# Optimization experiments

Hardware: AMD Instinct MI355X
Metric: run time of the kernel (lower is better)

The kernel has to match this reference:

```python
import math
import jax, jax.numpy as jnp
import numpy as np

B, C, E = 8, 2048, 1024

def setup_inputs() -> dict:
    key = jax.random.key(0)
    ks = jax.random.split(key, 7)
    s_e = 1.0 / math.sqrt(E)
    s_c = 1.0 / math.sqrt(C)
    return {
        'x': jax.random.normal(ks[0], (B, C, E), dtype=jnp.float32),
        'fc_w': jax.random.normal(ks[1], (E, E), dtype=jnp.float32) * s_e,
        'fc_b': jax.random.normal(ks[2], (E,), dtype=jnp.float32) * s_e,
        'alt_fc_w': jax.random.normal(ks[3], (C, C), dtype=jnp.float32) * s_c,
        'alt_fc_b': jax.random.normal(ks[4], (C,), dtype=jnp.float32) * s_c,
        'vfc_w': jax.random.normal(ks[5], (E, E), dtype=jnp.float32) * s_e,
        'vfc_b': jax.random.normal(ks[6], (E,), dtype=jnp.float32) * s_e,
    }

def reference(x, fc_w, fc_b, alt_fc_w, alt_fc_b, vfc_w, vfc_b):
    # y = fc(x): [b,c,e]
    y = jnp.einsum('bce,fe->bcf', x, fc_w) + fc_b
    # yx = alt_fc(x^T): [b,e,c] -> Linear over context dim -> [b,e,k]
    xx = jnp.swapaxes(x, 1, 2)                    # [b,e,c]
    yx = jnp.einsum('bec,kc->bek', xx, alt_fc_w) + alt_fc_b
    # attention scores: [b,c,k]
    attn = jnp.einsum('bce,bek->bck', y, yx)
    scale = 1.0 / math.sqrt(attn.shape[-1])
    attn = jax.nn.softmax(attn * scale, axis=-1)
    # values
    vx = jnp.einsum('bke,fe->bkf', x, vfc_w) + vfc_b
    out = jnp.einsum('bck,bke->bce', attn, vx)
    # post_feed=None -> return y only
    return out
```

## Files before the change

kernel.cpp:

```cpp
#include <hip/hip_runtime.h>
#include <stdint.h>

#define Bb 8
#define Cc 2048
#define Ee 1024

typedef unsigned short u16;
typedef __attribute__((ext_vector_type(8))) short short8;
typedef __attribute__((ext_vector_type(4))) float f32x4;

__device__ __forceinline__ u16 f2bf(float f){
    unsigned u = __builtin_bit_cast(unsigned, f);
    return (u16)((u + 0x7fffu + ((u >> 16) & 1u)) >> 16);
}
__device__ __forceinline__ float bf2f(u16 h){
    return __builtin_bit_cast(float, ((unsigned)h) << 16);
}
__device__ __forceinline__ void gld16(const void* g, void* l){
    __builtin_amdgcn_global_load_lds(
        (const __attribute__((address_space(1))) unsigned int*)g,
        (__attribute__((address_space(3))) unsigned int*)l,
        16, 0, 0);
}
#define MFMA(a,b,c) __builtin_amdgcn_mfma_f32_16x16x32_bf16((a),(b),(c),0,0,0)
#define SBAR()  __builtin_amdgcn_s_barrier()
#define SCHED0() __builtin_amdgcn_sched_barrier(0)
#define LGKM8() asm volatile("s_waitcnt lgkmcnt(8)" ::: "memory")
#define LGKM4() asm volatile("s_waitcnt lgkmcnt(4)" ::: "memory")
#define LGKM0() asm volatile("s_waitcnt lgkmcnt(0)" ::: "memory")
#define VMCNT0() asm volatile("s_waitcnt vmcnt(0)" ::: "memory")

__global__ __launch_bounds__(256) void k_cast_xt(const float* __restrict__ src,
                                                 u16* __restrict__ xb,
                                                 u16* __restrict__ xbT){
    __shared__ float tile[32][33];
    const int b = blockIdx.z;
    src += (long)b * Cc * Ee;
    xb  += (long)b * Cc * Ee;
    xbT += (long)b * Cc * Ee;
    const int c0 = blockIdx.x * 32;
    const int r0 = blockIdx.y * 32;
    const int tx = threadIdx.x & 31;
    const int ty = threadIdx.x >> 5;
    #pragma unroll
    for (int p = 0; p < 4; ++p){
        float v = src[(long)(r0 + ty + p*8) * Ee + c0 + tx];
        tile[ty + p*8][tx] = v;
        xb[(long)(r0 + ty + p*8) * Ee + c0 + tx] = f2bf(v);
    }
    __syncthreads();
    #pragma unroll
    for (int p = 0; p < 4; ++p)
        xbT[(long)(c0 + ty + p*8) * Cc + r0 + tx] = f2bf(tile[tx][ty + p*8]);
}

__global__ __launch_bounds__(256) void k_cast3(const float* __restrict__ s0, u16* __restrict__ d0, long n0,
                                               const float* __restrict__ s1, u16* __restrict__ d1, long n1,
                                               const float* __restrict__ s2, u16* __restrict__ d2, long n2){
    long i = (long)blockIdx.x * 256 + threadIdx.x;
    const long stride = (long)gridDim.x * 256;
    const long tot = n0 + n1 + n2;
    for (; i < tot; i += stride){
        const float* s; u16* d; long k;
        if (i < n0)          { s = s0; d = d0; k = i; }
        else if (i < n0 + n1){ s = s1; d = d1; k = i - n0; }
        else                 { s = s2; d = d2; k = i - n0 - n1; }
        float4 f = ((const float4*)s)[k];
        ((ushort4*)d)[k] = make_ushort4(f2bf(f.x), f2bf(f.y), f2bf(f.z), f2bf(f.w));
    }
}

template<int BIAS_MODE, int OUT_F32, int EPI, int PRIO>
__global__ __launch_bounds__(512, 2)
void k_gemm256(const u16* __restrict__ A, const u16* __restrict__ Bm,
               void* __restrict__ Cout, const float* __restrict__ bias,
               float* __restrict__ extra,
               int N, int K, long sA, long sB, long sC, float scale)
{
    __shared__ __attribute__((aligned(16))) char smem[131072];

    const int gx = gridDim.x, gy = gridDim.y;
    const int nwg = gx * gy * gridDim.z;
    const int lin = blockIdx.x + gx * (blockIdx.y + gy * blockIdx.z);
    const int swz = (lin & 7) * (nwg >> 3) + (lin >> 3);
    const int bx = swz % gx;
    const int tmp = swz / gx;
    const int by = tmp % gy;
    const int bz = tmp / gy;

    A  += (long)bz * sA;
    Bm += (long)bz * sB;
    u16*   Cm = (u16*)Cout + (OUT_F32 ? 0 : (long)bz * sC);
    float* Cf = (float*)Cout + (OUT_F32 ? (long)bz * sC : 0);

    const int tid  = threadIdx.x;
    const int lane = tid & 63;
    const int wave = tid >> 6;
    const int wr = wave >> 2;
    const int wc = wave & 3;
    const int tileM = bx * 256;
    const int tileN = by * 256;

    const int srow   = tid >> 3;
    const int schunk = (tid & 7) ^ (srow & 7);
    const u16* Ag = A  + (long)(tileM + srow) * K + schunk * 8;
    const u16* Bg = Bm + (long)(tileN + srow) * K + schunk * 8;
    const long uK = (long)64 * K;
    const int  ldst = tid * 16;

    const int lrow = lane & 15;
    const int lk   = lane >> 4;
    const int sw   = lrow & 7;
    const int cs0  = ((0 + lk) ^ sw) * 16;
    const int cs1  = ((4 + lk) ^ sw) * 16;
    const int arow0 = (wr*128 + lrow) * 128;
    const int brow0 = 32768 + (wc*64 + lrow) * 128;

    f32x4 acc[8][4];
    #pragma unroll
    for (int m = 0; m < 8; ++m)
        #pragma unroll
        for (int n = 0; n < 4; ++n)
            acc[m][n] = (f32x4){0.f,0.f,0.f,0.f};

    char* sm = smem;
    #pragma unroll
    for (int u = 0; u < 4; ++u) gld16(Bg + u*uK, sm + 32768 + u*8192 + ldst);
    #pragma unroll
    for (int u = 0; u < 4; ++u) gld16(Ag + u*uK, sm + u*8192 + ldst);
    __syncthreads();

    const int NT = K >> 6;
    short8 aE[4], aO[4], bE[4], bO[4];

    for (int t = 0; t < NT; ++t){
        const bool pref = (t + 1) < NT;
        char* cbuf = sm + ((t & 1) << 16);
        char* nbuf = sm + (((t + 1) & 1) << 16);
        const u16* Agt = Ag + (long)(t + 1) * 64;
        const u16* Bgt = Bg + (long)(t + 1) * 64;

        if (pref){
            gld16(Agt + 0*uK, nbuf + 0*8192 + ldst);
            gld16(Agt + 1*uK, nbuf + 1*8192 + ldst);
            gld16(Agt + 2*uK, nbuf + 2*8192 + ldst);
            gld16(Agt + 3*uK, nbuf + 3*8192 + ldst);
            gld16(Bgt + 0*uK, nbuf + 32768 + 0*8192 + ldst);
            gld16(Bgt + 1*uK, nbuf + 32768 + 1*8192 + ldst);
            gld16(Bgt + 2*uK, nbuf + 32768 + 2*8192 + ldst);
            gld16(Bgt + 3*uK, nbuf + 32768 + 3*8192 + ldst);
        }

        #pragma unroll
        for (int m = 0; m < 4; ++m) aE[m] = *(const short8*)(cbuf + arow0 + m*2048 + cs0);
        #pragma unroll
        for (int n = 0; n < 4; ++n) bE[n] = *(const short8*)(cbuf + brow0 + n*2048 + cs0);
        #pragma unroll
        for (int m = 0; m < 4; ++m) aO[m] = *(const short8*)(cbuf + arow0 + (m+4)*2048 + cs0);

        LGKM4(); SCHED0();
        if (PRIO) __builtin_amdgcn_s_setprio(1);
        #pragma unroll
        for (int m = 0; m < 4; ++m)
            #pragma unroll
            for (int n = 0; n < 4; ++n)
                acc[m][n] = MFMA(aE[m], bE[n], acc[m][n]);
        if (PRIO) __builtin_amdgcn_s_setprio(0);

        #pragma unroll
        for (int m = 0; m < 4; ++m) aE[m] = *(const short8*)(cbuf + arow0 + m*2048 + cs1);
        #pragma unroll
        for (int n = 0; n < 4; ++n) bO[n] = *(const short8*)(cbuf + brow0 + n*2048 + cs1);
        LGKM8(); SCHED0();
        if (PRIO) __builtin_amdgcn_s_setprio(1);
        #pragma unroll
        for (int m = 0; m < 4; ++m)
            #pragma unroll
            for (int n = 0; n < 4; ++n)
                acc[m+4][n] = MFMA(aO[m], bE[n], acc[m+4][n]);
        if (PRIO) __builtin_amdgcn_s_setprio(0);

        #pragma unroll
        for (int m = 0; m < 4; ++m) aO[m] = *(const short8*)(cbuf + arow0 + (m+4)*2048 + cs1);
        LGKM4(); SCHED0();
        if (PRIO) __builtin_amdgcn_s_setprio(1);
        #pragma unroll
        for (int m = 0; m < 4; ++m)
            #pragma unroll
            for (int n = 0; n < 4; ++n)
                acc[m][n] = MFMA(aE[m], bO[n], acc[m][n]);
        if (PRIO) __builtin_amdgcn_s_setprio(0);

        LGKM0(); SCHED0();
        if (PRIO) __builtin_amdgcn_s_setprio(1);
        #pragma unroll
        for (int m = 0; m < 4; ++m)
            #pragma unroll
            for (int n = 0; n < 4; ++n)
                acc[m+4][n] = MFMA(aO[m], bO[n], acc[m+4][n]);
        if (PRIO) __builtin_amdgcn_s_setprio(0);

        VMCNT0(); SBAR(); SCHED0();
    }

    const int r0base = tileM + wr*128 + lk*4;
    const int cbase  = tileN + wc*64 + lrow;

    if (EPI == 0){
        #pragma unroll
        for (int m = 0; m < 8; ++m){
            const int r0 = r0base + m*16;
            #pragma unroll
            for (int n = 0; n < 4; ++n){
                const int c = cbase + n*16;
                f32x4 v = acc[m][n];
                #pragma unroll
                for (int j = 0; j < 4; ++j){
                    float val = v[j] * scale;
                    if (BIAS_MODE == 1) val += bias[c];
                    if (BIAS_MODE == 2) val += bias[r0 + j];
                    if (OUT_F32) Cf[(long)(r0 + j) * N + c] = val;
                    else         Cm[(long)(r0 + j) * N + c] = f2bf(val);
                }
            }
        }
    } else if (EPI == 1){
        float* lsum = (float*)smem;
        const int rl0 = wr*128 + lk*4;
        #pragma unroll
        for (int m = 0; m < 8; ++m){
            const int r0 = r0base + m*16;
            #pragma unroll
            for (int j = 0; j < 4; ++j){
                float rp = 0.f;
                #pragma unroll
                for (int n = 0; n < 4; ++n){
                    float e = __expf(acc[m][n][j] * scale);
                    rp += e;
                    Cm[(long)(r0 + j) * N + (cbase + n*16)] = f2bf(e);
                }
                rp += __shfl_xor(rp, 1);
                rp += __shfl_xor(rp, 2);
                rp += __shfl_xor(rp, 4);
                rp += __shfl_xor(rp, 8);
                if (lrow == 0)
                    lsum[(rl0 + m*16 + j)*4 + wc] = rp;
            }
        }
        __syncthreads();
        if (tid < 256){
            float4 v4 = ((const float4*)lsum)[tid];
            extra[((long)bz*Cc + tileM + tid)*8 + by] = v4.x + v4.y + v4.z + v4.w;
        }
    } else {
        #pragma unroll
        for (int m = 0; m < 8; ++m){
            const int r0 = r0base + m*16;
            #pragma unroll
            for (int j = 0; j < 4; ++j){
                const float4* pr = (const float4*)(extra + ((long)bz*Cc + r0 + j)*8);
                float4 pa = pr[0], pb = pr[1];
                float S = pa.x+pa.y+pa.z+pa.w + pb.x+pb.y+pb.z+pb.w;
                const float inv = 1.f / S;
                #pragma unroll
                for (int n = 0; n < 4; ++n)
                    Cf[(long)(r0 + j) * N + (cbase + n*16)] = acc[m][n][j] * inv;
            }
        }
    }
}

extern "C" void kernel_launch(void* const* d_in, const int* in_sizes, int n_in,
                              void* d_out, int out_size, void* d_ws, size_t ws_size,
                              hipStream_t stream)
{
    const float* x     = (const float*)d_in[0];
    const float* fc_w  = (const float*)d_in[1];
    const float* fc_b  = (const float*)d_in[2];
    const float* altw  = (const float*)d_in[3];
    const float* altb  = (const float*)d_in[4];
    const float* vfc_w = (const float*)d_in[5];
    const float* vfc_b = (const float*)d_in[6];
    float* out = (float*)d_out;

    char* ws = (char*)d_ws;
    const size_t nBCE = (size_t)Bb * Cc * Ee;
    u16* xb   = (u16*)(ws);
    u16* xbT  = (u16*)(ws + 2 * nBCE);
    u16* P    = (u16*)(ws);
    u16* y    = (u16*)(ws + 4 * nBCE);
    u16* z    = (u16*)(ws + 6 * nBCE);
    u16* vxT  = (u16*)(ws + 8 * nBCE);
    u16* fcwb = (u16*)(ws + 10 * nBCE);
    u16* vfwb = fcwb + (size_t)Ee * Ee;
    u16* awb  = vfwb + (size_t)Ee * Ee;
    float* rpart = (float*)(ws + 10 * nBCE);

    k_cast_xt<<<dim3(Ee / 32, Cc / 32, Bb), 256, 0, stream>>>(x, xb, xbT);
    k_cast3<<<2048, 256, 0, stream>>>(fc_w, fcwb, (long)Ee * Ee / 4,
                                      vfc_w, vfwb, (long)Ee * Ee / 4,
                                      altw, awb, (long)Cc * Cc / 4);

    const long sBCE = (long)Cc * Ee;
    const long sBCC = (long)Cc * Cc;
    dim3 blk(512);

    k_gemm256<1, 0, 0, 1><<<dim3(Cc/256, Ee/256, Bb), blk, 0, stream>>>(
        xb, fcwb, y, fc_b, nullptr, Ee, Ee, sBCE, 0, sBCE, 1.f);

    k_gemm256<2, 0, 0, 1><<<dim3(Ee/256, Cc/256, Bb), blk, 0, stream>>>(
        vfwb, xb, vxT, vfc_b, nullptr, Cc, Ee, 0, sBCE, sBCE, 1.f);

    k_gemm256<2, 0, 0, 0><<<dim3(Cc/256, Ee/256, Bb), blk, 0, stream>>>(
        awb, xbT, z, altb, nullptr, Ee, Cc, 0, sBCE, sBCE, 1.f);

    k_gemm256<0, 0, 1, 1><<<dim3(Cc/256, Cc/256, Bb), blk, 0, stream>>>(
        y, z, P, nullptr, rpart, Cc, Ee, sBCE, sBCE, sBCC, 0.022097086912079608f);

    k_gemm256<0, 1, 2, 0><<<dim3(Cc/256, Ee/256, Bb), blk, 0, stream>>>(
        P, vxT, out, nullptr, rpart, Ee, Cc, sBCC, sBCE, sBCE, 1.f);
}
```

Baseline: 309.1 us.

## Merge prep casts and batch the three projection GEMMs into one launch

Folds the x cast/transpose kernel and the weight-cast kernel into a single prep launch. The three independent projection GEMMs (alt_fc, fc, vfc) now run as one grouped launch of 768 workgroups driven by a segment descriptor, so there are fewer launches and fewer partially filled waves. The template specialisations are replaced by runtime segment fields, and the s_setprio hints are removed. The row-sum buffer moves so it no longer overlaps the bf16 weight copies. The cost is runtime branching in the epilogue and possibly weaker compiler specialisation.

```diff
diff --git a/kernel.cpp b/kernel.cpp
--- a/kernel.cpp
+++ b/kernel.cpp
@@ -12,9 +12,6 @@
 __device__ __forceinline__ u16 f2bf(float f){
     unsigned u = __builtin_bit_cast(unsigned, f);
     return (u16)((u + 0x7fffu + ((u >> 16) & 1u)) >> 16);
-}
-__device__ __forceinline__ float bf2f(u16 h){
-    return __builtin_bit_cast(float, ((unsigned)h) << 16);
 }
 __device__ __forceinline__ void gld16(const void* g, void* l){
     __builtin_amdgcn_global_load_lds(
@@ -30,68 +27,85 @@
 #define LGKM0() asm volatile("s_waitcnt lgkmcnt(0)" ::: "memory")
 #define VMCNT0() asm volatile("s_waitcnt vmcnt(0)" ::: "memory")
 
-__global__ __launch_bounds__(256) void k_cast_xt(const float* __restrict__ src,
-                                                 u16* __restrict__ xb,
-                                                 u16* __restrict__ xbT){
+struct Seg {
+    const u16* A; const u16* Bm; void* C; const float* bias; float* extra;
+    int N, K, gx, gy;
+    long sA, sB, sC;
+    float scale;
+    int bias_mode;
+    int epi;
+    int out_f32;
+};
+struct Desc { Seg s0, s1, s2; int n0, n1; };
+
+__global__ __launch_bounds__(256) void k_prep(const float* __restrict__ x,
+                                              u16* __restrict__ xb, u16* __restrict__ xbT,
+                                              const float* __restrict__ fw, u16* __restrict__ fwb,
+                                              const float* __restrict__ vw, u16* __restrict__ vwb,
+                                              const float* __restrict__ aw, u16* __restrict__ awb){
     __shared__ float tile[32][33];
-    const int b = blockIdx.z;
-    src += (long)b * Cc * Ee;
-    xb  += (long)b * Cc * Ee;
-    xbT += (long)b * Cc * Ee;
-    const int c0 = blockIdx.x * 32;
-    const int r0 = blockIdx.y * 32;
-    const int tx = threadIdx.x & 31;
-    const int ty = threadIdx.x >> 5;
-    #pragma unroll
-    for (int p = 0; p < 4; ++p){
-        float v = src[(long)(r0 + ty + p*8) * Ee + c0 + tx];
-        tile[ty + p*8][tx] = v;
-        xb[(long)(r0 + ty + p*8) * Ee + c0 + tx] = f2bf(v);
+    const int blk = blockIdx.x;
+    if (blk < 16384){
+        const int cx = blk & 31;
+        const int rest = blk >> 5;
+        const int cy = rest & 63;
+        const int b  = rest >> 6;
+        const float* src = x + (long)b * Cc * Ee;
+        u16* xbp  = xb  + (long)b * Cc * Ee;
+        u16* xbTp = xbT + (long)b * Cc * Ee;
+        const int c0 = cx * 32;
+        const int r0 = cy * 32;
+        const int tx = threadIdx.x & 31;
+        const int ty = threadIdx.x >> 5;
+        #pragma unroll
+        for (int p = 0; p < 4; ++p){
+            float v = src[(long)(r0 + ty + p*8) * Ee + c0 + tx];
+            tile[ty + p*8][tx] = v;
+            xbp[(long)(r0 + ty + p*8) * Ee + c0 + tx] = f2bf(v);
+        }
+        __syncthreads();
+        #pragma unroll
+        for (int p = 0; p < 4; ++p)
+            xbTp[(long)(c0 + ty + p*8) * Cc + r0 + tx] = f2bf(tile[tx][ty + p*8]);
+    } else {
+        const long n0 = (long)Ee * Ee / 4, n1 = n0, n2 = (long)Cc * Cc / 4;
+        long i = (long)(blk - 16384) * 256 + threadIdx.x;
+        const long stride = 2048L * 256;
+        const long tot = n0 + n1 + n2;
+        for (; i < tot; i += stride){
+            const float* s; u16* d; long k;
+            if (i < n0)          { s = fw; d = fwb; k = i; }
+            else if (i < n0 + n1){ s = vw; d = vwb; k = i - n0; }
+            else                 { s = aw; d = awb; k = i - n0 - n1; }
+            float4 f = ((const float4*)s)[k];
+            ((ushort4*)d)[k] = make_ushort4(f2bf(f.x), f2bf(f.y), f2bf(f.z), f2bf(f.w));
+        }
     }
-    __syncthreads();
-    #pragma unroll
-    for (int p = 0; p < 4; ++p)
-        xbT[(long)(c0 + ty + p*8) * Cc + r0 + tx] = f2bf(tile[tx][ty + p*8]);
-}
-
-__global__ __launch_bounds__(256) void k_cast3(const float* __restrict__ s0, u16* __restrict__ d0, long n0,
-                                               const float* __restrict__ s1, u16* __restrict__ d1, long n1,
-                                               const float* __restrict__ s2, u16* __restrict__ d2, long n2){
-    long i = (long)blockIdx.x * 256 + threadIdx.x;
-    const long stride = (long)gridDim.x * 256;
-    const long tot = n0 + n1 + n2;
-    for (; i < tot; i += stride){
-        const float* s; u16* d; long k;
-        if (i < n0)          { s = s0; d = d0; k = i; }
-        else if (i < n0 + n1){ s = s1; d = d1; k = i - n0; }
-        else                 { s = s2; d = d2; k = i - n0 - n1; }
-        float4 f = ((const float4*)s)[k];
-        ((ushort4*)d)[k] = make_ushort4(f2bf(f.x), f2bf(f.y), f2bf(f.z), f2bf(f.w));
-    }
-}
-
-template<int BIAS_MODE, int OUT_F32, int EPI, int PRIO>
+}
+
 __global__ __launch_bounds__(512, 2)
-void k_gemm256(const u16* __restrict__ A, const u16* __restrict__ Bm,
-               void* __restrict__ Cout, const float* __restrict__ bias,
-               float* __restrict__ extra,
-               int N, int K, long sA, long sB, long sC, float scale)
+void k_gemm_multi(Desc d)
 {
     __shared__ __attribute__((aligned(16))) char smem[131072];
 
-    const int gx = gridDim.x, gy = gridDim.y;
-    const int nwg = gx * gy * gridDim.z;
-    const int lin = blockIdx.x + gx * (blockIdx.y + gy * blockIdx.z);
+    const int blk = (int)blockIdx.x;
+    Seg S; int lin;
+    if (blk < d.n0)            { S = d.s0; lin = blk; }
+    else if (blk < d.n0 + d.n1){ S = d.s1; lin = blk - d.n0; }
+    else                       { S = d.s2; lin = blk - d.n0 - d.n1; }
+
+    const int nwg = S.gx * S.gy * Bb;
     const int swz = (lin & 7) * (nwg >> 3) + (lin >> 3);
-    const int bx = swz % gx;
-    const int tmp = swz / gx;
-    const int by = tmp % gy;
-    const int bz = tmp / gy;
-
-    A  += (long)bz * sA;
-    Bm += (long)bz * sB;
-    u16*   Cm = (u16*)Cout + (OUT_F32 ? 0 : (long)bz * sC);
-    float* Cf = (float*)Cout + (OUT_F32 ? (long)bz * sC : 0);
+    const int bx = swz % S.gx;
+    const int tmp = swz / S.gx;
+    const int by = tmp % S.gy;
+    const int bz = tmp / S.gy;
+
+    const u16* A  = S.A  + (long)bz * S.sA;
+    const u16* Bm = S.Bm + (long)bz * S.sB;
+    const int  N = S.N, K = S.K;
+    u16*   Cm = (u16*)S.C + (long)bz * S.sC;
+    float* Cf = (float*)S.C + (long)bz * S.sC;
 
     const int tid  = threadIdx.x;
     const int lane = tid & 63;
@@ -159,46 +173,38 @@
         for (int m = 0; m < 4; ++m) aO[m] = *(const short8*)(cbuf + arow0 + (m+4)*2048 + cs0);
 
         LGKM4(); SCHED0();
-        if (PRIO) __builtin_amdgcn_s_setprio(1);
         #pragma unroll
         for (int m = 0; m < 4; ++m)
             #pragma unroll
             for (int n = 0; n < 4; ++n)
                 acc[m][n] = MFMA(aE[m], bE[n], acc[m][n]);
-        if (PRIO) __builtin_amdgcn_s_setprio(0);
 
         #pragma unroll
         for (int m = 0; m < 4; ++m) aE[m] = *(const short8*)(cbuf + arow0 + m*2048 + cs1);
         #pragma unroll
         for (int n = 0; n < 4; ++n) bO[n] = *(const short8*)(cbuf + brow0 + n*2048 + cs1);
         LGKM8(); SCHED0();
-        if (PRIO) __builtin_amdgcn_s_setprio(1);
         #pragma unroll
         for (int m = 0; m < 4; ++m)
             #pragma unroll
             for (int n = 0; n < 4; ++n)
                 acc[m+4][n] = MFMA(aO[m], bE[n], acc[m+4][n]);
-        if (PRIO) __builtin_amdgcn_s_setprio(0);
 
         #pragma unroll
         for (int m = 0; m < 4; ++m) aO[m] = *(const short8*)(cbuf + arow0 + (m+4)*2048 + cs1);
         LGKM4(); SCHED0();
-        if (PRIO) __builtin_amdgcn_s_setprio(1);
         #pragma unroll
         for (int m = 0; m < 4; ++m)
             #pragma unroll
             for (int n = 0; n < 4; ++n)
                 acc[m][n] = MFMA(aE[m], bO[n], acc[m][n]);
-        if (PRIO) __builtin_amdgcn_s_setprio(0);
 
         LGKM0(); SCHED0();
-        if (PRIO) __builtin_amdgcn_s_setprio(1);
         #pragma unroll
         for (int m = 0; m < 4; ++m)
             #pragma unroll
             for (int n = 0; n < 4; ++n)
                 acc[m+4][n] = MFMA(aO[m], bO[n], acc[m+4][n]);
-        if (PRIO) __builtin_amdgcn_s_setprio(0);
 
         VMCNT0(); SBAR(); SCHED0();
     }
@@ -206,7 +212,8 @@
     const int r0base = tileM + wr*128 + lk*4;
     const int cbase  = tileN + wc*64 + lrow;
 
-    if (EPI == 0){
+    if (S.epi == 0){
+        const float scale = S.scale;
         #pragma unroll
         for (int m = 0; m < 8; ++m){
             const int r0 = r0base + m*16;
@@ -217,14 +224,15 @@
                 #pragma unroll
                 for (int j = 0; j < 4; ++j){
                     float val = v[j] * scale;
-                    if (BIAS_MODE == 1) val += bias[c];
-                    if (BIAS_MODE == 2) val += bias[r0 + j];
-                    if (OUT_F32) Cf[(long)(r0 + j) * N + c] = val;
-                    else         Cm[(long)(r0 + j) * N + c] = f2bf(val);
+                    if (S.bias_mode == 1) val += S.bias[c];
+                    if (S.bias_mode == 2) val += S.bias[r0 + j];
+                    if (S.out_f32) Cf[(long)(r0 + j) * N + c] = val;
+                    else           Cm[(long)(r0 + j) * N + c] = f2bf(val);
                 }
             }
         }
-    } else if (EPI == 1){
+    } else if (S.epi == 1){
+        const float scale = S.scale;
         float* lsum = (float*)smem;
         const int rl0 = wr*128 + lk*4;
         #pragma unroll
@@ -250,7 +258,7 @@
         __syncthreads();
         if (tid < 256){
             float4 v4 = ((const float4*)lsum)[tid];
-            extra[((long)bz*Cc + tileM + tid)*8 + by] = v4.x + v4.y + v4.z + v4.w;
+            S.extra[((long)bz*Cc + tileM + tid)*8 + by] = v4.x + v4.y + v4.z + v4.w;
         }
     } else {
         #pragma unroll
@@ -258,10 +266,10 @@
             const int r0 = r0base + m*16;
             #pragma unroll
             for (int j = 0; j < 4; ++j){
-                const float4* pr = (const float4*)(extra + ((long)bz*Cc + r0 + j)*8);
+                const float4* pr = (const float4*)(S.extra + ((long)bz*Cc + r0 + j)*8);
                 float4 pa = pr[0], pb = pr[1];
-                float S = pa.x+pa.y+pa.z+pa.w + pb.x+pb.y+pb.z+pb.w;
-                const float inv = 1.f / S;
+                float Ssum = pa.x+pa.y+pa.z+pa.w + pb.x+pb.y+pb.z+pb.w;
+                const float inv = 1.f / Ssum;
                 #pragma unroll
                 for (int n = 0; n < 4; ++n)
                     Cf[(long)(r0 + j) * N + (cbase + n*16)] = acc[m][n][j] * inv;
@@ -294,29 +302,29 @@
     u16* fcwb = (u16*)(ws + 10 * nBCE);
     u16* vfwb = fcwb + (size_t)Ee * Ee;
     u16* awb  = vfwb + (size_t)Ee * Ee;
-    float* rpart = (float*)(ws + 10 * nBCE);
-
-    k_cast_xt<<<dim3(Ee / 32, Cc / 32, Bb), 256, 0, stream>>>(x, xb, xbT);
-    k_cast3<<<2048, 256, 0, stream>>>(fc_w, fcwb, (long)Ee * Ee / 4,
-                                      vfc_w, vfwb, (long)Ee * Ee / 4,
-                                      altw, awb, (long)Cc * Cc / 4);
+    float* rpart = (float*)(ws + 10 * nBCE + 2*((size_t)Ee*Ee*2 + (size_t)Cc*Cc));
 
     const long sBCE = (long)Cc * Ee;
     const long sBCC = (long)Cc * Cc;
-    dim3 blk(512);
-
-    k_gemm256<1, 0, 0, 1><<<dim3(Cc/256, Ee/256, Bb), blk, 0, stream>>>(
-        xb, fcwb, y, fc_b, nullptr, Ee, Ee, sBCE, 0, sBCE, 1.f);
-
-    k_gemm256<2, 0, 0, 1><<<dim3(Ee/256, Cc/256, Bb), blk, 0, stream>>>(
-        vfwb, xb, vxT, vfc_b, nullptr, Cc, Ee, 0, sBCE, sBCE, 1.f);
-
-    k_gemm256<2, 0, 0, 0><<<dim3(Cc/256, Ee/256, Bb), blk, 0, stream>>>(
-        awb, xbT, z, altb, nullptr, Ee, Cc, 0, sBCE, sBCE, 1.f);
-
-    k_gemm256<0, 0, 1, 1><<<dim3(Cc/256, Cc/256, Bb), blk, 0, stream>>>(
-        y, z, P, nullptr, rpart, Cc, Ee, sBCE, sBCE, sBCC, 0.022097086912079608f);
-
-    k_gemm256<0, 1, 2, 0><<<dim3(Cc/256, Ee/256, Bb), blk, 0, stream>>>(
-        P, vxT, out, nullptr, rpart, Ee, Cc, sBCC, sBCE, sBCE, 1.f);
-}
+
+    k_prep<<<18432, 256, 0, stream>>>(x, xb, xbT, fc_w, fcwb, vfc_w, vfwb, altw, awb);
+
+    Desc d1;
+    d1.s0 = Seg{ awb, xbT, z, altb, nullptr, Ee, Cc, 8, 4, 0, sBCE, sBCE, 1.f, 2, 0, 0 };
+    d1.s1 = Seg{ xb, fcwb, y, fc_b, nullptr, Ee, Ee, 8, 4, sBCE, 0, sBCE, 1.f, 1, 0, 0 };
+    d1.s2 = Seg{ vfwb, xb, vxT, vfc_b, nullptr, Cc, Ee, 4, 8, 0, sBCE, sBCE, 1.f, 2, 0, 0 };
+    d1.n0 = 256; d1.n1 = 256;
+    k_gemm_multi<<<768, 512, 0, stream>>>(d1);
+
+    Desc d2;
+    d2.s0 = Seg{ y, z, P, nullptr, rpart, Cc, Ee, 8, 8, sBCE, sBCE, sBCC, 0.022097086912079608f, 0, 1, 0 };
+    d2.s1 = d2.s0; d2.s2 = d2.s0;
+    d2.n0 = 512; d2.n1 = 0;
+    k_gemm_multi<<<512, 512, 0, stream>>>(d2);
+
+    Desc d3;
+    d3.s0 = Seg{ P, vxT, out, nullptr, rpart, Ee, Cc, 8, 4, sBCC, sBCE, sBCE, 1.f, 0, 2, 1 };
+    d3.s1 = d3.s0; d3.s2 = d3.s0;
+    d3.n0 = 256; d3.n1 = 0;
+    k_gemm_multi<<<256, 512, 0, stream>>>(d3);
+}
```

Result: slower. 353.7 us (+14.5%).
